# Kernel tuning notes

Measured on AMD Instinct MI355X. Metric: run time of the kernel, lower is better.

## Reference

```python
import jax, jax.numpy as jnp
import numpy as np

N_NODES = 50000
N_EDGES = 800000
IN_DIM = 128
EMB = 64
EDGE_DIM = 6
N_LAYERS = 4
OUT_DIM = 1


def setup_inputs() -> dict:
    key = jax.random.key(0)
    ks = jax.random.split(key, 20)
    s = 0.05
    inp = {
        "x": jax.random.normal(ks[0], (N_NODES, IN_DIM), jnp.float32),
        "edge_index": jax.random.randint(ks[1], (2, N_EDGES), 0, N_NODES, jnp.int64),
        "edge_attr": jax.random.normal(ks[2], (N_EDGES, EDGE_DIM), jnp.float32),
        # input projection
        "lin_in_w": jax.random.normal(ks[3], (IN_DIM, EMB), jnp.float32) * s,
        "lin_in_b": jnp.zeros((EMB,), jnp.float32),
        # stacked per-layer MLP params: message MLP psi: (2*EMB+EDGE_DIM)->EMB->EMB
        "msg_w1": jax.random.normal(ks[4], (N_LAYERS, 2 * EMB + EDGE_DIM, EMB), jnp.float32) * s,
        "msg_b1": jnp.zeros((N_LAYERS, EMB), jnp.float32),
        "msg_w2": jax.random.normal(ks[5], (N_LAYERS, EMB, EMB), jnp.float32) * s,
        "msg_b2": jnp.zeros((N_LAYERS, EMB), jnp.float32),
        # update MLP phi: (2*EMB)->EMB->EMB
        "upd_w1": jax.random.normal(ks[6], (N_LAYERS, 2 * EMB, EMB), jnp.float32) * s,
        "upd_b1": jnp.zeros((N_LAYERS, EMB), jnp.float32),
        "upd_w2": jax.random.normal(ks[7], (N_LAYERS, EMB, EMB), jnp.float32) * s,
        "upd_b2": jnp.zeros((N_LAYERS, EMB), jnp.float32),
        # output head
        "pred_w": jax.random.normal(ks[8], (EMB, OUT_DIM), jnp.float32) * s,
        "pred_b": jnp.zeros((OUT_DIM,), jnp.float32),
    }
    return inp


def reference(x, edge_index, edge_attr, lin_in_w, lin_in_b,
              msg_w1, msg_b1, msg_w2, msg_b2,
              upd_w1, upd_b1, upd_w2, upd_b2,
              pred_w, pred_b):
    n = x.shape[0]
    src = edge_index[0]  # h_j: source nodes
    dst = edge_index[1]  # h_i: target nodes (aggregation index in PyG default flow)
    h = x @ lin_in_w + lin_in_b  # (n, EMB)
    n_layers = msg_w1.shape[0]
    for l in range(n_layers):
        # message: psi([h_i, h_j, e_ij])  -> (E, EMB)
        m = jnp.concatenate([h[dst], h[src], edge_attr], axis=-1)
        m = jax.nn.relu(m @ msg_w1[l] + msg_b1[l])
        m = jax.nn.relu(m @ msg_w2[l] + msg_b2[l])
        # aggregate: scatter-add over target nodes
        agg = jax.ops.segment_sum(m, dst, num_segments=n)
        # update: phi([h, m_i]) with residual connection (h = h + conv(h))
        u = jnp.concatenate([h, agg], axis=-1)
        u = jax.nn.relu(u @ upd_w1[l] + upd_b1[l])
        u = jax.nn.relu(u @ upd_w2[l] + upd_b2[l])
        h = h + u
    out = h @ pred_w + pred_b  # (n, OUT_DIM)
    return jnp.sum(out, axis=-2)  # (OUT_DIM,)
```

## Files before the change

### kernel.cpp

```cpp
#include <hip/hip_runtime.h>
#include <hip/hip_fp16.h>


typedef __attribute__((ext_vector_type(8))) short short8;
typedef __attribute__((ext_vector_type(4))) float float4v;

__device__ __forceinline__ unsigned short f2bf(float f) {
    unsigned int u = __float_as_uint(f);
    unsigned int r = u + 0x7fff + ((u >> 16) & 1);
    return (unsigned short)(r >> 16);
}
__device__ __forceinline__ float bf2f(unsigned short u) {
    return __uint_as_float(((unsigned int)u) << 16);
}
__device__ __forceinline__ __half2 u2h2(unsigned int u) {
    union { unsigned int u; __half2 h; } c; c.u = u; return c.h;
}
__device__ __forceinline__ unsigned int h22u(__half2 h) {
    union { unsigned int u; __half2 h; } c; c.h = h; return c.u;
}
__device__ __forceinline__ unsigned int pkmax0(unsigned int a) {
    unsigned int r;
    asm("v_pk_max_f16 %0, %1, %2" : "=v"(r) : "v"(a), "v"(0u));
    return r;
}

#define MFMA16(a, b, c)  __builtin_amdgcn_mfma_f32_16x16x32_bf16(a, b, c, 0, 0, 0)
#define MFMA16H(a, b, c) __builtin_amdgcn_mfma_f32_16x16x32_f16(a, b, c, 0, 0, 0)

struct bfpair { short hi, lo; };
__device__ __forceinline__ bfpair wsplit(float wv) {
    bfpair p;
    unsigned short h = f2bf(wv);
    float hf = __uint_as_float(((unsigned int)h) << 16);
    p.hi = (short)h;
    p.lo = (short)f2bf(wv - hf);
    return p;
}

#define WP_TOTAL 106496
#define OFF_IN   0
#define OFF_PRE(l)  (8192  + (l) * 8192)
#define OFF_MW2(l)  (40960 + (l) * 4096)
#define OFF_UW1(l)  (57344 + (l) * 8192)
#define OFF_UW2(l)  (90112 + (l) * 4096)

__global__ __launch_bounds__(256) void k_wprep(const float* __restrict__ lin_w,
        const float* __restrict__ mw1, const float* __restrict__ mw2,
        const float* __restrict__ uw1, const float* __restrict__ uw2,
        unsigned short* __restrict__ H, unsigned short* __restrict__ L) {
    const int tid = blockIdx.x * 256 + threadIdx.x;
    if (tid >= WP_TOTAL) return;
    float val;
    if (tid < 8192) {
        int rem = tid;
        int nt = rem >> 11, kf = (rem >> 9) & 3;
        int lane = (rem >> 3) & 63, j = rem & 7;
        int k = kf * 32 + (lane >> 4) * 8 + j;
        val = lin_w[k * 64 + nt * 16 + (lane & 15)];
    } else if (tid < 40960) {
        int t = tid - 8192, layer = t >> 13, rem = t & 8191;
        int nt = rem >> 10, kf = (rem >> 9) & 1;
        int lane = (rem >> 3) & 63, j = rem & 7;
        int k = kf * 32 + (lane >> 4) * 8 + j;
        const float* w1 = mw1 + (size_t)layer * 134 * 64;
        val = (nt < 4) ? w1[k * 64 + nt * 16 + (lane & 15)]
                       : w1[(64 + k) * 64 + (nt - 4) * 16 + (lane & 15)];
    } else if (tid < 57344) {
        int t = tid - 40960, layer = t >> 12, rem = t & 4095;
        int nt = rem >> 10, kf = (rem >> 9) & 1;
        int lane = (rem >> 3) & 63, j = rem & 7;
        int k = kf * 32 + (lane >> 4) * 8 + j;
        val = mw2[(size_t)layer * 4096 + k * 64 + nt * 16 + (lane & 15)];
    } else if (tid < 90112) {
        int t = tid - 57344, layer = t >> 13, rem = t & 8191;
        int nt = rem >> 11, kf = (rem >> 9) & 3;
        int lane = (rem >> 3) & 63, j = rem & 7;
        int k = kf * 32 + (lane >> 4) * 8 + j;
        val = uw1[(size_t)layer * 8192 + k * 64 + nt * 16 + (lane & 15)];
    } else {
        int t = tid - 90112, layer = t >> 12, rem = t & 4095;
        int nt = rem >> 10, kf = (rem >> 9) & 1;
        int lane = (rem >> 3) & 63, j = rem & 7;
        int k = kf * 32 + (lane >> 4) * 8 + j;
        val = uw2[(size_t)layer * 4096 + k * 64 + nt * 16 + (lane & 15)];
    }
    if (tid >= 40960 && tid < 57344) {
        __half hh = __float2half_rn(val);
        float hf = __half2float(hh);
        __half hl = __float2half_rn(val - hf);
        H[tid] = __half_as_ushort(hh);
        L[tid] = __half_as_ushort(hl);
    } else {
        bfpair p = wsplit(val);
        H[tid] = (unsigned short)p.hi;
        L[tid] = (unsigned short)p.lo;
    }
}

#define LOADFRAG(dst, arr, nt, KF, kf) \
    dst = *(const short8*)&arr[((((nt) * (KF)) + (kf)) * 64 + lane) * 8]

__global__ __launch_bounds__(256) void k_hist(const int* __restrict__ dst,
        int* __restrict__ deg, int nEdges) {
    int e = blockIdx.x * blockDim.x + threadIdx.x;
    if (e < nEdges) atomicAdd(&deg[dst[e]], 1);
}

__global__ __launch_bounds__(256) void k_scan1(const int* __restrict__ deg,
        int* __restrict__ local, int* __restrict__ bsum, int nNodes) {
    __shared__ int sm[256];
    const int t = threadIdx.x;
    const int n = blockIdx.x * 256 + t;
    int v = (n < nNodes) ? deg[n] : 0;
    sm[t] = v;
    __syncthreads();
    for (int off = 1; off < 256; off <<= 1) {
        int u = (t >= off) ? sm[t - off] : 0;
        __syncthreads();
        sm[t] += u;
        __syncthreads();
    }
    if (n < nNodes) local[n] = sm[t] - v;
    if (t == 255) bsum[blockIdx.x] = sm[255];
}

__global__ __launch_bounds__(256) void k_scan2(int* __restrict__ bsum, int nB) {
    __shared__ int sm[256];
    const int t = threadIdx.x;
    int v = (t < nB) ? bsum[t] : 0;
    sm[t] = v;
    __syncthreads();
    for (int off = 1; off < 256; off <<= 1) {
        int u = (t >= off) ? sm[t - off] : 0;
        __syncthreads();
        sm[t] += u;
        __syncthreads();
    }
    if (t < nB) bsum[t] = sm[t] - v;
}

__global__ __launch_bounds__(256) void k_scan3(const int* __restrict__ local,
        const int* __restrict__ bsum, int* __restrict__ cursor, int nNodes) {
    int n = blockIdx.x * 256 + threadIdx.x;
    if (n < nNodes) cursor[n] = bsum[blockIdx.x] + local[n];
}

__global__ __launch_bounds__(256) void k_scatter(const int* __restrict__ src,
        const int* __restrict__ dst, const float* __restrict__ ea,
        int* __restrict__ cursor, float* __restrict__ rec, int nEdges) {
    int e = blockIdx.x * blockDim.x + threadIdx.x;
    if (e < nEdges) {
        int d = dst[e];
        int s = src[e];
        int pos = atomicAdd(&cursor[d], 1);
        const float* p = ea + (size_t)e * 6;
        float4 lo, hi;
        lo.x = __int_as_float(s);
        lo.y = __int_as_float(d);
        lo.z = p[0];
        lo.w = p[1];
        hi.x = p[2];
        hi.y = p[3];
        hi.z = p[4];
        hi.w = p[5];
        float4* q = (float4*)(rec + (size_t)pos * 8);
        q[0] = lo;
        q[1] = hi;
    }
}


__global__ __launch_bounds__(256) void k_in(const float* __restrict__ x,
        const unsigned short* __restrict__ wh, const unsigned short* __restrict__ wl,
        const float* __restrict__ bia, float* __restrict__ h, int nNodes) {
    const int lane = threadIdx.x & 63;
    const int wib  = threadIdx.x >> 6;
    const int quad = lane >> 4, col = lane & 15;
    __shared__ unsigned short sm[4][16 * 136];
    unsigned short* __restrict__ mt = sm[wib];

    short8 bh[4][4], bl[4][4];
#pragma unroll
    for (int nt = 0; nt < 4; ++nt)
#pragma unroll
        for (int kf = 0; kf < 4; ++kf) {
            LOADFRAG(bh[nt][kf], wh, nt, 4, kf);
            LOADFRAG(bl[nt][kf], wl, nt, 4, kf);
        }
    float bv[4];
#pragma unroll
    for (int nt = 0; nt < 4; ++nt) bv[nt] = bia[nt * 16 + col];

    const int nTiles = (nNodes + 15) >> 4;
    const int wid = blockIdx.x * 4 + wib;
    const int nw  = gridDim.x * 4;
    for (int tile = wid; tile < nTiles; tile += nw) {
        const int base = tile * 16;
#pragma unroll
        for (int j = 0; j < 16; ++j) {
            int row = min(base + j, nNodes - 1);
            mt[j * 136 + lane]      = f2bf(x[(size_t)row * 128 + lane]);
            mt[j * 136 + 64 + lane] = f2bf(x[(size_t)row * 128 + 64 + lane]);
        }
        __builtin_amdgcn_s_waitcnt(0);
        short8 a[4];
#pragma unroll
        for (int kf = 0; kf < 4; ++kf)
            a[kf] = *(const short8*)&mt[col * 136 + kf * 32 + quad * 8];
#pragma unroll
        for (int nt = 0; nt < 4; ++nt) {
            float4v c = {0.f, 0.f, 0.f, 0.f};
#pragma unroll
            for (int kf = 0; kf < 4; ++kf) c = MFMA16(a[kf], bh[nt][kf], c);
#pragma unroll
            for (int kf = 0; kf < 4; ++kf) c = MFMA16(a[kf], bl[nt][kf], c);
#pragma unroll
            for (int r = 0; r < 4; ++r) {
                int row = base + quad * 4 + r;
                if (row < nNodes)
                    h[(size_t)row * 64 + nt * 16 + col] = c[r] + bv[nt];
            }
        }
    }
}

__global__ __launch_bounds__(256) void k_pre(const float* __restrict__ h,
        const unsigned short* __restrict__ wh, const unsigned short* __restrict__ wl,
        const float* __restrict__ b1m,
        unsigned short* __restrict__ P, unsigned short* __restrict__ Q,
        int nNodes) {
    const int lane = threadIdx.x & 63;
    const int wib  = threadIdx.x >> 6;
    const int quad = lane >> 4, col = lane & 15;
    __shared__ unsigned short sm[4][16 * 72];
    unsigned short* __restrict__ mt = sm[wib];

    short8 bh[8][2], bl[8][2];
#pragma unroll
    for (int nt = 0; nt < 8; ++nt)
#pragma unroll
        for (int kf = 0; kf < 2; ++kf) {
            LOADFRAG(bh[nt][kf], wh, nt, 2, kf);
            LOADFRAG(bl[nt][kf], wl, nt, 2, kf);
        }
    float bv1[4];
#pragma unroll
    for (int nt = 0; nt < 4; ++nt) bv1[nt] = b1m[nt * 16 + col];

    const int nTiles = (nNodes + 15) >> 4;
    const int wid = blockIdx.x * 4 + wib;
    const int nw  = gridDim.x * 4;
    for (int tile = wid; tile < nTiles; tile += nw) {
        const int base = tile * 16;
#pragma unroll
        for (int j = 0; j < 16; ++j) {
            int row = min(base + j, nNodes - 1);
            mt[j * 72 + lane] = f2bf(h[(size_t)row * 64 + lane]);
        }
        __builtin_amdgcn_s_waitcnt(0);
        short8 a0 = *(const short8*)&mt[col * 72 + quad * 8];
        short8 a1 = *(const short8*)&mt[col * 72 + 32 + quad * 8];
#pragma unroll
        for (int nt = 0; nt < 8; ++nt) {
            float4v c = {0.f, 0.f, 0.f, 0.f};
            c = MFMA16(a0, bh[nt][0], c);
            c = MFMA16(a1, bh[nt][1], c);
            c = MFMA16(a0, bl[nt][0], c);
            c = MFMA16(a1, bl[nt][1], c);
            unsigned short* __restrict__ outp = (nt < 4) ? P : Q;
            const int nc = (nt & 3) * 16 + col;
            const float badd = (nt < 4) ? bv1[nt & 3] : 0.f;
#pragma unroll
            for (int r = 0; r < 4; ++r) {
                int row = base + quad * 4 + r;
                if (row < nNodes)
                    outp[(size_t)row * 64 + nc] =
                        __half_as_ushort(__float2half_rn(c[r] + badd));
            }
        }
    }
}

__global__ __launch_bounds__(256) void k_upd(float* __restrict__ h,
        float* __restrict__ agg,
        const unsigned short* __restrict__ wh1, const unsigned short* __restrict__ wl1,
        const float* __restrict__ b1,
        const unsigned short* __restrict__ wh2, const unsigned short* __restrict__ wl2,
        const float* __restrict__ b2,
        const unsigned short* __restrict__ whP, const unsigned short* __restrict__ wlP,
        const float* __restrict__ b1m,
        unsigned short* __restrict__ P, unsigned short* __restrict__ Q,
        float* __restrict__ colsum,
        int nNodes, int doCS, int doPre) {
    const int lane = threadIdx.x & 63;
    const int wib  = threadIdx.x >> 6;
    const int quad = lane >> 4, col = lane & 15;
    __shared__ unsigned short sm[4][16 * 136];
    __shared__ unsigned short tb[4][16 * 72];
    __shared__ unsigned short wB[8192];
    __shared__ unsigned short wP[8192];
    unsigned short* __restrict__ mt = sm[wib];
    unsigned short* __restrict__ tv = tb[wib];

    {
        const short8* __restrict__ sH = (const short8*)wh2;
        const short8* __restrict__ sL = (const short8*)wl2;
        short8* __restrict__ dB = (short8*)wB;
        for (int i = threadIdx.x; i < 512; i += 256) {
            dB[i]       = sH[i];
            dB[512 + i] = sL[i];
        }
        if (doPre) {
            const short8* __restrict__ pH = (const short8*)whP;
            const short8* __restrict__ pL = (const short8*)wlP;
            short8* __restrict__ dP = (short8*)wP;
            for (int i = threadIdx.x; i < 1024; i += 256) {
                short8 hi8 = pH[i], lo8 = pL[i], o;
#pragma unroll
                for (int e = 0; e < 8; ++e) {
                    float w = bf2f((unsigned short)hi8[e]) +
                              bf2f((unsigned short)lo8[e]);
                    o[e] = (short)__half_as_ushort(__float2half_rn(w));
                }
                dP[i] = o;
            }
        }
    }
    __syncthreads();

    short8 bh[4][4], bl[4][4];
#pragma unroll
    for (int nt = 0; nt < 4; ++nt)
#pragma unroll
        for (int kf = 0; kf < 4; ++kf) {
            LOADFRAG(bh[nt][kf], wh1, nt, 4, kf);
            LOADFRAG(bl[nt][kf], wl1, nt, 4, kf);
        }
    float bv1[4], bv2[4], bvP[4];
#pragma unroll
    for (int nt = 0; nt < 4; ++nt) {
        bv1[nt] = b1[nt * 16 + col];
        bv2[nt] = b2[nt * 16 + col];
        bvP[nt] = b1m[nt * 16 + col];
    }

    float cs0 = 0.f, cs1 = 0.f, cs2 = 0.f, cs3 = 0.f;
    const int nTiles = (nNodes + 15) >> 4;
    const int wid = blockIdx.x * 4 + wib;
    const int nw  = gridDim.x * 4;
    for (int tile = wid; tile < nTiles; tile += nw) {
        const int base = tile * 16;
#pragma unroll
        for (int j = 0; j < 16; ++j) {
            int row = min(base + j, nNodes - 1);
            mt[j * 136 + lane]      = f2bf(h[(size_t)row * 64 + lane]);
            mt[j * 136 + 64 + lane] = f2bf(agg[(size_t)row * 64 + lane]);
        }
        __builtin_amdgcn_s_waitcnt(0);
#pragma unroll
        for (int j = 0; j < 16; ++j) {
            int row = base + j;
            if (row < nNodes) agg[(size_t)row * 64 + lane] = 0.f;
        }
        short8 a[4];
#pragma unroll
        for (int kf = 0; kf < 4; ++kf)
            a[kf] = *(const short8*)&mt[col * 136 + kf * 32 + quad * 8];
#pragma unroll
        for (int nt = 0; nt < 4; ++nt) {
            float4v c = {0.f, 0.f, 0.f, 0.f};
#pragma unroll
            for (int kf = 0; kf < 4; ++kf) c = MFMA16(a[kf], bh[nt][kf], c);
#pragma unroll
            for (int kf = 0; kf < 4; ++kf) c = MFMA16(a[kf], bl[nt][kf], c);
#pragma unroll
            for (int r = 0; r < 4; ++r)
                tv[(quad * 4 + r) * 72 + nt * 16 + col] =
                    f2bf(fmaxf(c[r] + bv1[nt], 0.f));
        }
        __builtin_amdgcn_s_waitcnt(0);
        short8 a0 = *(const short8*)&tv[col * 72 + quad * 8];
        short8 a1 = *(const short8*)&tv[col * 72 + 32 + quad * 8];
#pragma unroll
        for (int nt = 0; nt < 4; ++nt) {
            const short8 h0 = *(const short8*)&wB[((nt * 2 + 0) * 64 + lane) * 8];
            const short8 h1 = *(const short8*)&wB[((nt * 2 + 1) * 64 + lane) * 8];
            const short8 l0 = *(const short8*)&wB[4096 + ((nt * 2 + 0) * 64 + lane) * 8];
            const short8 l1 = *(const short8*)&wB[4096 + ((nt * 2 + 1) * 64 + lane) * 8];
            float4v c = {0.f, 0.f, 0.f, 0.f};
            c = MFMA16(a0, h0, c);
            c = MFMA16(a1, h1, c);
            c = MFMA16(a0, l0, c);
            c = MFMA16(a1, l1, c);
#pragma unroll
            for (int r = 0; r < 4; ++r) {
                int row = base + quad * 4 + r;
                if (row < nNodes) {
                    float* hp = &h[(size_t)row * 64 + nt * 16 + col];
                    float hn = *hp + fmaxf(c[r] + bv2[nt], 0.f);
                    *hp = hn;
                    if (doPre)
                        tv[(quad * 4 + r) * 72 + nt * 16 + col] =
                            __half_as_ushort(__float2half_rn(hn));
                    cs0 += (nt == 0) ? hn : 0.f;
                    cs1 += (nt == 1) ? hn : 0.f;
                    cs2 += (nt == 2) ? hn : 0.f;
                    cs3 += (nt == 3) ? hn : 0.f;
                }
            }
        }
        if (doPre) {
            __builtin_amdgcn_s_waitcnt(0);
            short8 p0 = *(const short8*)&tv[col * 72 + quad * 8];
            short8 p1 = *(const short8*)&tv[col * 72 + 32 + quad * 8];
#pragma unroll
            for (int nt = 0; nt < 8; ++nt) {
                const short8 f0 = *(const short8*)&wP[((nt * 2 + 0) * 64 + lane) * 8];
                const short8 f1 = *(const short8*)&wP[((nt * 2 + 1) * 64 + lane) * 8];
                float4v c = {0.f, 0.f, 0.f, 0.f};
                c = MFMA16H(p0, f0, c);
                c = MFMA16H(p1, f1, c);
                unsigned short* __restrict__ outp = (nt < 4) ? P : Q;
                const int nc = (nt & 3) * 16 + col;
                const float badd = (nt < 4) ? bvP[nt & 3] : 0.f;
#pragma unroll
                for (int r = 0; r < 4; ++r) {
                    int row = base + quad * 4 + r;
                    if (row < nNodes)
                        outp[(size_t)row * 64 + nc] =
                            __half_as_ushort(__float2half_rn(c[r] + badd));
                }
            }
        }
    }
    if (doCS) {
        cs0 += __shfl_xor(cs0, 16); cs0 += __shfl_xor(cs0, 32);
        cs1 += __shfl_xor(cs1, 16); cs1 += __shfl_xor(cs1, 32);
        cs2 += __shfl_xor(cs2, 16); cs2 += __shfl_xor(cs2, 32);
        cs3 += __shfl_xor(cs3, 16); cs3 += __shfl_xor(cs3, 32);
        const float tot = (quad == 0) ? cs0 : (quad == 1) ? cs1
                        : (quad == 2) ? cs2 : cs3;
        atomicAdd(&colsum[lane], tot);
    }
}

#define EST 72

__global__ __launch_bounds__(256, 4) void k_edge(const unsigned short* __restrict__ P,
        const unsigned short* __restrict__ Q, const float* __restrict__ rec,
        const float* __restrict__ w1e,
        const unsigned short* __restrict__ wh, const unsigned short* __restrict__ wl,
        const float* __restrict__ b2,
        float* __restrict__ agg, int nEdges) {
    const int lane = threadIdx.x & 63;
    const int wib  = threadIdx.x >> 6;
    const int wid  = blockIdx.x * 4 + wib;
    const int nw   = gridDim.x * 4;
    const int quad = lane >> 4;
    const int col  = lane & 15;
    const int li   = lane & 31;
    const int hs   = lane >> 5;

    __shared__ unsigned short m1b[4][32 * EST];
    __shared__ unsigned int   eab[4][256];
    __shared__ unsigned short wB[8192];
    unsigned short* __restrict__ mt  = m1b[wib];
    unsigned int*   __restrict__ eaw = eab[wib];

    {
        const short8* __restrict__ sH = (const short8*)wh;
        const short8* __restrict__ sL = (const short8*)wl;
        short8* __restrict__ dB = (short8*)wB;
        for (int i = threadIdx.x; i < 512; i += 256) {
            dB[i]       = sH[i];
            dB[512 + i] = sL[i];
        }
    }
    __syncthreads();

    __half2 w1ec2[6];
#pragma unroll
    for (int jj = 0; jj < 6; ++jj)
        w1ec2[jj] = __halves2half2(__float2half_rn(w1e[jj * 64 + 2 * li]),
                                   __float2half_rn(w1e[jj * 64 + 2 * li + 1]));

    float b2v[4];
#pragma unroll
    for (int nt = 0; nt < 4; ++nt) b2v[nt] = b2[nt * 16 + col];

    const int nBatch = (nEdges + 31) >> 5;
    const int per = nBatch / nw, rem = nBatch % nw;
    const int btLo = wid * per + min(wid, rem);
    const int btHi = btLo + per + (wid < rem ? 1 : 0);

    const int* __restrict__ reci = (const int*)rec;

    for (int bt = btLo; bt < btHi; ++bt) {
        const int base = __builtin_amdgcn_readfirstlane(bt << 5);
        const int gidx = min(base + li, nEdges - 1);
        const int vsj = reci[(size_t)gidx * 8];
        const int vdj = reci[(size_t)gidx * 8 + 1];
        const int vprev = __shfl_up(vdj, 1);
        unsigned long long bmask =
            __ballot(lane < 32 && (li == 0 || vdj != vprev));
        bmask |= (1ull << 32) | 1ull;

        const int fMax = nEdges * 8 - 1;
        const int fBase = base * 8;
#pragma unroll
        for (int k = 0; k < 4; ++k)
            eaw[k * 64 + lane] =
                h22u(__float2half2_rn(rec[min(fBase + k * 64 + lane, fMax)]));

#pragma unroll
        for (int j = 0; j < 16; ++j) {
            const int d0 = __builtin_amdgcn_readlane(vdj, 2 * j);
            const int d1 = __builtin_amdgcn_readlane(vdj, 2 * j + 1);
            const int s0 = __builtin_amdgcn_readlane(vsj, 2 * j);
            const int s1 = __builtin_amdgcn_readlane(vsj, 2 * j + 1);
            const int d = hs ? d1 : d0;
            const int s = hs ? s1 : s0;
            const int rsel = 2 * j + hs;
            const unsigned int p2 = *(const unsigned int*)&P[(size_t)d * 64 + 2 * li];
            const unsigned int q2 = *(const unsigned int*)&Q[(size_t)s * 64 + 2 * li];
            __half2 t = __hadd2(u2h2(p2), u2h2(q2));
#pragma unroll
            for (int jj = 0; jj < 6; ++jj) {
                const unsigned int eu = eaw[16 * j + 8 * hs + 2 + jj];
                t = __hfma2(u2h2(eu), w1ec2[jj], t);
            }
            *(unsigned int*)((char*)mt + rsel * (EST * 2) + li * 4) = pkmax0(h22u(t));
        }
        __builtin_amdgcn_s_waitcnt(0);

        short8 a00 = *(const short8*)&mt[col * EST + quad * 8];
        short8 a01 = *(const short8*)&mt[col * EST + 32 + quad * 8];
        short8 a10 = *(const short8*)&mt[(16 + col) * EST + quad * 8];
        short8 a11 = *(const short8*)&mt[(16 + col) * EST + 32 + quad * 8];

        float4v m2v[2][4];
#pragma unroll
        for (int nt = 0; nt < 4; ++nt) {
            const short8 h0 = *(const short8*)&wB[((nt * 2 + 0) * 64 + lane) * 8];
            const short8 h1 = *(const short8*)&wB[((nt * 2 + 1) * 64 + lane) * 8];
            const short8 l0 = *(const short8*)&wB[4096 + ((nt * 2 + 0) * 64 + lane) * 8];
            const short8 l1 = *(const short8*)&wB[4096 + ((nt * 2 + 1) * 64 + lane) * 8];
            float4v c0 = {0.f, 0.f, 0.f, 0.f};
            float4v c1 = {0.f, 0.f, 0.f, 0.f};
            c0 = MFMA16H(a00, h0, c0);
            c0 = MFMA16H(a01, h1, c0);
            c0 = MFMA16H(a00, l0, c0);
            c0 = MFMA16H(a01, l1, c0);
            c1 = MFMA16H(a10, h0, c1);
            c1 = MFMA16H(a11, h1, c1);
            c1 = MFMA16H(a10, l0, c1);
            c1 = MFMA16H(a11, l1, c1);
#pragma unroll
            for (int r = 0; r < 4; ++r) {
                const bool v0 = base + (quad * 4 + r) < nEdges;
                const bool v1 = base + 16 + (quad * 4 + r) < nEdges;
                m2v[0][nt][r] = v0 ? fmaxf(c0[r] + b2v[nt], 0.f) : 0.f;
                m2v[1][nt][r] = v1 ? fmaxf(c1[r] + b2v[nt], 0.f) : 0.f;
            }
        }

        int r0 = 0;
        while (r0 < 32) {
            const int nid = __builtin_amdgcn_readlane(vdj, r0);
            const int r1 = r0 + 1 + (int)__builtin_ctzll(bmask >> (r0 + 1));
            float s0 = 0.f, s1 = 0.f, s2 = 0.f, s3 = 0.f;
#pragma unroll
            for (int t = 0; t < 2; ++t)
#pragma unroll
                for (int r = 0; r < 4; ++r) {
                    const int R = t * 16 + quad * 4 + r;
                    const bool in = (R >= r0) && (R < r1);
                    s0 += in ? m2v[t][0][r] : 0.f;
                    s1 += in ? m2v[t][1][r] : 0.f;
                    s2 += in ? m2v[t][2][r] : 0.f;
                    s3 += in ? m2v[t][3][r] : 0.f;
                }
            s0 += __shfl_xor(s0, 16); s0 += __shfl_xor(s0, 32);
            s1 += __shfl_xor(s1, 16); s1 += __shfl_xor(s1, 32);
            s2 += __shfl_xor(s2, 16); s2 += __shfl_xor(s2, 32);
            s3 += __shfl_xor(s3, 16); s3 += __shfl_xor(s3, 32);
            const float tot = (quad == 0) ? s0 : (quad == 1) ? s1
                            : (quad == 2) ? s2 : s3;
            atomicAdd(&agg[(size_t)nid * 64 + lane], tot);
            r0 = r1;
        }
    }
}

__global__ void k_out(const float* __restrict__ colsum, const float* __restrict__ pw,
                      const float* __restrict__ pb, float* __restrict__ out, int nNodes) {
    const int lane = threadIdx.x;
    float v = colsum[lane] * pw[lane];
#pragma unroll
    for (int off = 32; off; off >>= 1) v += __shfl_down(v, off);
    if (lane == 0) out[0] = v + (float)nNodes * pb[0];
}

extern "C" void kernel_launch(void* const* d_in, const int* in_sizes, int n_in,
                              void* d_out, int out_size, void* d_ws, size_t ws_size,
                              hipStream_t stream) {
    const float* x     = (const float*)d_in[0];
    const int*   ei    = (const int*)d_in[1];
    const float* ea    = (const float*)d_in[2];
    const float* lin_w = (const float*)d_in[3];
    const float* lin_b = (const float*)d_in[4];
    const float* mw1   = (const float*)d_in[5];
    const float* mb1   = (const float*)d_in[6];
    const float* mw2   = (const float*)d_in[7];
    const float* mb2   = (const float*)d_in[8];
    const float* uw1   = (const float*)d_in[9];
    const float* ub1   = (const float*)d_in[10];
    const float* uw2   = (const float*)d_in[11];
    const float* ub2   = (const float*)d_in[12];
    const float* pw    = (const float*)d_in[13];
    const float* pb    = (const float*)d_in[14];

    const int nNodes = in_sizes[0] / 128;
    const int nEdges = in_sizes[1] / 2;
    const int* src = ei;
    const int* dst = ei + nEdges;

    float* h       = (float*)d_ws;
    float* agg     = h   + (size_t)nNodes * 64;
    float* rec     = agg + (size_t)nNodes * 64;
    float* colsum  = rec + (size_t)nEdges * 8;
    unsigned short* Pb  = (unsigned short*)(colsum + 64);
    unsigned short* Qb  = Pb + (size_t)nNodes * 64;
    unsigned short* wpH = Qb + (size_t)nNodes * 64;
    unsigned short* wpL = wpH + WP_TOTAL;
    int*   deg     = (int*)(wpL + WP_TOTAL);
    int*   cursor  = deg + nNodes;
    int*   local   = cursor + nNodes;
    int*   bsum    = local + nNodes;

    const int NB_T    = 392;
    const int NB_EDGE = 2048;
    const int NB_FLAT = (nEdges + 255) / 256;
    const int NB_SCAN = (nNodes + 255) / 256;

    hipMemsetAsync(deg, 0, (size_t)nNodes * sizeof(int), stream);
    hipMemsetAsync(colsum, 0, 64 * sizeof(float), stream);
    hipMemsetAsync(agg, 0, (size_t)nNodes * 64 * sizeof(float), stream);
    k_hist<<<NB_FLAT, 256, 0, stream>>>(dst, deg, nEdges);
    k_scan1<<<NB_SCAN, 256, 0, stream>>>(deg, local, bsum, nNodes);
    k_scan2<<<1, 256, 0, stream>>>(bsum, NB_SCAN);
    k_scan3<<<NB_SCAN, 256, 0, stream>>>(local, bsum, cursor, nNodes);
    k_scatter<<<NB_FLAT, 256, 0, stream>>>(src, dst, ea, cursor, rec, nEdges);
    k_wprep<<<(WP_TOTAL + 255) / 256, 256, 0, stream>>>(lin_w, mw1, mw2, uw1, uw2, wpH, wpL);

    k_in<<<NB_T, 256, 0, stream>>>(x, wpH + OFF_IN, wpL + OFF_IN, lin_b, h, nNodes);
    k_pre<<<NB_T, 256, 0, stream>>>(h, wpH + OFF_PRE(0), wpL + OFF_PRE(0),
        mb1, Pb, Qb, nNodes);

    for (int l = 0; l < 4; ++l) {
        const int lp = (l < 3) ? (l + 1) : 3;
        k_edge<<<NB_EDGE, 256, 0, stream>>>(Pb, Qb, rec,
            mw1 + (size_t)l * 134 * 64 + 128 * 64,
            wpH + OFF_MW2(l), wpL + OFF_MW2(l), mb2 + l * 64, agg, nEdges);
        k_upd<<<NB_T, 256, 0, stream>>>(h, agg,
            wpH + OFF_UW1(l), wpL + OFF_UW1(l), ub1 + l * 64,
            wpH + OFF_UW2(l), wpL + OFF_UW2(l), ub2 + l * 64,
            wpH + OFF_PRE(lp), wpL + OFF_PRE(lp),
            (l < 3) ? (mb1 + (l + 1) * 64) : mb1,
            Pb, Qb, colsum, nNodes, (l == 3) ? 1 : 0, (l < 3) ? 1 : 0);
    }

    k_out<<<1, 64, 0, stream>>>(colsum, pw, pb, (float*)d_out, nNodes);
}
```

Measured before the change: 526.1 us.

## Prefetch next tile's h/agg rows into registers and narrow waits to LDS

The node-update loop now loads the next tile's h and agg rows into registers while the current tile is being computed, so global-load latency overlaps with the MFMA work. The full s_waitcnt(0) calls are replaced with lgkmcnt(0) waits plus a scheduling barrier, so LDS synchronization no longer waits on outstanding global loads. This adds 32 registers per lane and could lower occupancy. The prefetch of agg happens after the current tile's agg rows are zeroed, but it reads different rows, so ordering stays correct.

```diff
diff --git a/kernel.cpp b/kernel.cpp
--- a/kernel.cpp
+++ b/kernel.cpp
@@ -23,6 +23,10 @@
     unsigned int r;
     asm("v_pk_max_f16 %0, %1, %2" : "=v"(r) : "v"(a), "v"(0u));
     return r;
+}
+__device__ __forceinline__ void lgkm_drain() {
+    asm volatile("s_waitcnt lgkmcnt(0)" ::: "memory");
+    __builtin_amdgcn_sched_barrier(0);
 }
 
 #define MFMA16(a, b, c)  __builtin_amdgcn_mfma_f32_16x16x32_bf16(a, b, c, 0, 0, 0)
@@ -349,20 +353,41 @@
     const int nTiles = (nNodes + 15) >> 4;
     const int wid = blockIdx.x * 4 + wib;
     const int nw  = gridDim.x * 4;
+
+    float hv[16], av[16];
+    if (wid < nTiles) {
+        const int base = wid * 16;
+#pragma unroll
+        for (int j = 0; j < 16; ++j) {
+            int row = min(base + j, nNodes - 1);
+            hv[j] = h[(size_t)row * 64 + lane];
+            av[j] = agg[(size_t)row * 64 + lane];
+        }
+    }
+
     for (int tile = wid; tile < nTiles; tile += nw) {
         const int base = tile * 16;
 #pragma unroll
         for (int j = 0; j < 16; ++j) {
-            int row = min(base + j, nNodes - 1);
-            mt[j * 136 + lane]      = f2bf(h[(size_t)row * 64 + lane]);
-            mt[j * 136 + 64 + lane] = f2bf(agg[(size_t)row * 64 + lane]);
-        }
-        __builtin_amdgcn_s_waitcnt(0);
+            mt[j * 136 + lane]      = f2bf(hv[j]);
+            mt[j * 136 + 64 + lane] = f2bf(av[j]);
+        }
 #pragma unroll
         for (int j = 0; j < 16; ++j) {
             int row = base + j;
             if (row < nNodes) agg[(size_t)row * 64 + lane] = 0.f;
         }
+        const int nxt = tile + nw;
+        if (nxt < nTiles) {
+            const int nb = nxt * 16;
+#pragma unroll
+            for (int j = 0; j < 16; ++j) {
+                int row = min(nb + j, nNodes - 1);
+                hv[j] = h[(size_t)row * 64 + lane];
+                av[j] = agg[(size_t)row * 64 + lane];
+            }
+        }
+        lgkm_drain();
         short8 a[4];
 #pragma unroll
         for (int kf = 0; kf < 4; ++kf)
@@ -379,7 +404,7 @@
                 tv[(quad * 4 + r) * 72 + nt * 16 + col] =
                     f2bf(fmaxf(c[r] + bv1[nt], 0.f));
         }
-        __builtin_amdgcn_s_waitcnt(0);
+        lgkm_drain();
         short8 a0 = *(const short8*)&tv[col * 72 + quad * 8];
         short8 a1 = *(const short8*)&tv[col * 72 + 32 + quad * 8];
 #pragma unroll
@@ -411,7 +436,7 @@
             }
         }
         if (doPre) {
-            __builtin_amdgcn_s_waitcnt(0);
+            lgkm_drain();
             short8 p0 = *(const short8*)&tv[col * 72 + quad * 8];
             short8 p1 = *(const short8*)&tv[col * 72 + 32 + quad * 8];
 #pragma unroll
```

After: 516.5 us. About the same (-1.8%).
